# Optimization experiments

Hardware: AMD Instinct MI355X
Metric: run time of the kernel (lower is better)

The kernel has to match this reference:

```python
import jax, jax.numpy as jnp
import numpy as np

B, S, H, DK = 8, 2048, 1024, 64


def setup_inputs() -> dict:
    key = jax.random.key(0)
    ks = jax.random.split(key, 8)
    x = jax.random.normal(ks[0], (B, S, H), dtype=jnp.float32)
    # padding at the tail: positions >= length are pad (True)
    lengths = jax.random.randint(ks[1], (B,), S // 2, S + 1)
    padding_mask = jnp.arange(S)[None, :] >= lengths[:, None]  # [B,S] bool, True = pad
    sc = 1.0 / np.sqrt(H)
    Wq = jax.random.normal(ks[2], (H, DK), dtype=jnp.float32) * sc
    Wk = jax.random.normal(ks[3], (H, DK), dtype=jnp.float32) * sc
    Wv = jax.random.normal(ks[4], (H, DK), dtype=jnp.float32) * sc
    bq = jnp.zeros((DK,), dtype=jnp.float32)
    bk = jnp.zeros((DK,), dtype=jnp.float32)
    bv = jnp.zeros((DK,), dtype=jnp.float32)
    return {"x": x, "padding_mask": padding_mask, "Wq": Wq, "bq": bq,
            "Wk": Wk, "bk": bk, "Wv": Wv, "bv": bv}


def reference(x, padding_mask, Wq, bq, Wk, bk, Wv, bv):
    # Single-head attention, dropout_pe = 0 (identity), masking=True (causal).
    d_k = Wq.shape[-1]
    Q = jnp.einsum('bsh,hd->bsd', x, Wq) + bq
    K = jnp.einsum('bsh,hd->bsd', x, Wk) + bk
    V = jnp.einsum('bsh,hd->bsd', x, Wv) + bv
    scores = jnp.einsum('bqd,bkd->bqk', Q, K) / jnp.sqrt(jnp.asarray(d_k, x.dtype))
    neg_inf = jnp.finfo(scores.dtype).min
    # padding mask over keys: [B,1,S]
    scores = jnp.where(padding_mask[:, None, :], neg_inf, scores)
    # causal mask: strictly upper triangular is disallowed
    seq = scores.shape[-1]
    causal = jnp.triu(jnp.ones((seq, seq), dtype=bool), k=1)
    scores = jnp.where(causal[None, :, :], neg_inf, scores)
    W = jax.nn.softmax(scores, axis=-1)
    # zero out attention rows for padded query positions: [B,S,1]
    W = jnp.where(padding_mask[:, :, None], 0.0, W)
    return jnp.einsum('bqk,bkd->bqd', W, V)
```

## Files before the change

### kernel.cpp

```cpp
#include <hip/hip_runtime.h>
#include <hip/hip_bf16.h>

#define NB 8
#define SEQ 2048
#define HD 1024
#define DK 64

#define QSCALE 0.1803368801111244f
#define FIXMAX2 11.541560327111708f

typedef __attribute__((ext_vector_type(4))) float f32x4;
typedef __attribute__((ext_vector_type(8))) short bf16x8;
typedef __attribute__((ext_vector_type(4))) unsigned short u16x4;

__device__ __forceinline__ short f2bf(float f) {
    union { float f; unsigned u; } v; v.f = f;
    unsigned r = v.u + 0x7fffu + ((v.u >> 16) & 1u);
    return (short)(r >> 16);
}
__device__ __forceinline__ bf16x8 pack8(f32x4 v0, f32x4 v1) {
    union { bf16x8 v; __hip_bfloat162 h[4]; } u;
    u.h[0] = __float22bfloat162_rn(make_float2(v0[0], v0[1]));
    u.h[1] = __float22bfloat162_rn(make_float2(v0[2], v0[3]));
    u.h[2] = __float22bfloat162_rn(make_float2(v1[0], v1[1]));
    u.h[3] = __float22bfloat162_rn(make_float2(v1[2], v1[3]));
    return u.v;
}

__global__ void prep_kernel(const unsigned* __restrict__ mask,
                            const float* __restrict__ Wq, const float* __restrict__ Wk,
                            const float* __restrict__ Wv,
                            int* __restrict__ lengths, short* __restrict__ Wp) {
    if (blockIdx.x < 768) {
        int idx = blockIdx.x * 256 + threadIdx.x;
        int j = idx & 7, lane = (idx >> 3) & 63;
        int slot = idx >> 9;
        int fr = slot % 3, q2 = slot / 3;
        int kh = q2 & 1, cg = (q2 >> 1) & 3, kbg = q2 >> 3;
        int g = lane >> 4, c = lane & 15;
        int n = cg * 3 + fr;
        int m = n >> 2, colm = (n & 3) * 16 + c;
        int k = kbg * 64 + kh * 32 + g * 8 + j;
        const float* W = (m == 0) ? Wq : (m == 1) ? Wk : Wv;
        Wp[idx] = f2bf(W[(size_t)k * DK + colm]);
        return;
    }
    __shared__ int sdet;
    __shared__ int scnt;
    int b = blockIdx.x - 768, t = threadIdx.x;
    if (t == 0) { sdet = 0; scnt = 0; }
    __syncthreads();
    int det = 0;
    for (int i = t; i < 4096; i += 256) {
        unsigned w = mask[i];
        if (w > 1u && w != 0x3F800000u) det = 1;
    }
    if (det) atomicOr(&sdet, 1);
    __syncthreads();
    int cnt = 0;
    if (sdet) {
        const unsigned char* m8 = (const unsigned char*)mask;
        for (int s = t; s < SEQ; s += 256) cnt += (m8[b * SEQ + s] == 0) ? 1 : 0;
    } else {
        for (int s = t; s < SEQ; s += 256) cnt += (mask[b * SEQ + s] == 0u) ? 1 : 0;
    }
    atomicAdd(&scnt, cnt);
    __syncthreads();
    if (t == 0) lengths[b] = scnt;
}

__global__ __launch_bounds__(256, 3) void qkv_kernel(
    const float* __restrict__ x,
    const float* __restrict__ bq, const float* __restrict__ bk, const float* __restrict__ bv,
    const short* __restrict__ Wp,
    short* __restrict__ Q, short* __restrict__ K, short* __restrict__ Vt) {
    __shared__ float xs[2][32][64];
    int t = threadIdx.x;
    int cg = t >> 6, lane = t & 63;
    int g = lane >> 4, c = lane & 15;
    int r0 = blockIdx.x * 32;
    int bb = r0 >> 11, sbase = r0 & (SEQ - 1);

    int srow = t >> 3, sc8 = t & 7;
    const float* xsrc = x + (size_t)(r0 + srow) * HD + sc8 * 8;
    float* wbase = &xs[0][0][0];
    int wo0 = srow * 64 + (((2 * sc8) ^ (srow & 15)) << 2);
    int wo1 = srow * 64 + (((2 * sc8 + 1) ^ (srow & 15)) << 2);

    const short* wpw = Wp + (size_t)cg * 3072 + (size_t)lane * 8;

    f32x4 z = {0.f, 0.f, 0.f, 0.f};
    f32x4 acc[2][3];
    #pragma unroll
    for (int rf = 0; rf < 2; rf++)
        #pragma unroll
        for (int fr = 0; fr < 3; fr++) acc[rf][fr] = z;

    {
        f32x4 x0 = *(const f32x4*)xsrc;
        f32x4 x1 = *(const f32x4*)(xsrc + 4);
        *(f32x4*)(wbase + wo0) = x0;
        *(f32x4*)(wbase + wo1) = x1;
    }
    bf16x8 Bc[2][3];
    #pragma unroll
    for (int kh = 0; kh < 2; kh++)
        #pragma unroll
        for (int fr = 0; fr < 3; fr++)
            Bc[kh][fr] = *(const bf16x8*)(wpw + kh * 1536 + fr * 512);
    f32x4 nxA0 = *(const f32x4*)(xsrc + 64);
    f32x4 nxA1 = *(const f32x4*)(xsrc + 68);
    __syncthreads();

    const float* rbase0 = &xs[0][0][0] + c * 64;
    #pragma unroll
    for (int kbg = 0; kbg < 16; kbg++) {
        int cur = kbg & 1;
        f32x4 nxB0, nxB1;
        bf16x8 Bn[2][3];
        if (kbg < 14) {
            const float* p = xsrc + (kbg + 2) * 64;
            nxB0 = *(const f32x4*)p;
            nxB1 = *(const f32x4*)(p + 4);
        }
        if (kbg < 15) {
            #pragma unroll
            for (int kh = 0; kh < 2; kh++)
                #pragma unroll
                for (int fr = 0; fr < 3; fr++)
                    Bn[kh][fr] = *(const bf16x8*)(wpw + (kbg + 1) * 12288 + kh * 1536 + fr * 512);
        }
        bf16x8 Af[2][2];
        #pragma unroll
        for (int rf = 0; rf < 2; rf++)
            #pragma unroll
            for (int kh = 0; kh < 2; kh++) {
                const float* rp = rbase0 + cur * 2048 + rf * 1024;
                int lg = kh * 8 + 2 * g;
                f32x4 lo = *(const f32x4*)(rp + ((lg ^ c) << 2));
                f32x4 hi = *(const f32x4*)(rp + (((lg + 1) ^ c) << 2));
                Af[rf][kh] = pack8(lo, hi);
            }
        #pragma unroll
        for (int kh = 0; kh < 2; kh++)
            #pragma unroll
            for (int fr = 0; fr < 3; fr++)
                #pragma unroll
                for (int rf = 0; rf < 2; rf++)
                    acc[rf][fr] = __builtin_amdgcn_mfma_f32_16x16x32_bf16(Af[rf][kh], Bc[kh][fr], acc[rf][fr], 0, 0, 0);
        if (kbg < 15) {
            float* wb = wbase + (cur ^ 1) * 2048;
            *(f32x4*)(wb + wo0) = nxA0;
            *(f32x4*)(wb + wo1) = nxA1;
            #pragma unroll
            for (int kh = 0; kh < 2; kh++)
                #pragma unroll
                for (int fr = 0; fr < 3; fr++) Bc[kh][fr] = Bn[kh][fr];
        }
        if (kbg < 14) { nxA0 = nxB0; nxA1 = nxB1; }
        __syncthreads();
    }

    #pragma unroll
    for (int rf = 0; rf < 2; rf++)
        #pragma unroll
        for (int fr = 0; fr < 3; fr++) {
            int n = cg * 3 + fr;
            int m = n >> 2, colm = (n & 3) * 16 + c;
            const float* bias = (m == 0) ? bq : (m == 1) ? bk : bv;
            float bv_ = bias[colm];
            if (m == 2) {
                u16x4 pk;
                #pragma unroll
                for (int j = 0; j < 4; j++) pk[j] = (unsigned short)f2bf(acc[rf][fr][j] + bv_);
                int srw = sbase + rf * 16 + 4 * g;
                *(u16x4*)(Vt + (size_t)bb * DK * SEQ + (size_t)colm * SEQ + srw) = pk;
            } else {
                #pragma unroll
                for (int j = 0; j < 4; j++) {
                    int row = r0 + rf * 16 + 4 * g + j;
                    float s = acc[rf][fr][j] + bv_;
                    if (m == 0) Q[(size_t)row * DK + colm] = f2bf(s * QSCALE);
                    else        K[(size_t)row * DK + colm] = f2bf(s);
                }
            }
        }
}

__global__ __launch_bounds__(256) void attn_kernel(
    const short* __restrict__ Q, const short* __restrict__ K_, const short* __restrict__ Vt,
    const int* __restrict__ lengths, float* __restrict__ out) {
    __shared__ float macc[4][32][66];
    __shared__ float ll[4][32];
    short* plds = (short*)&macc[0][0][0];

    int bid = blockIdx.x;
    int qt = 63 - (bid & 63);
    int b = bid >> 6;
    int len = lengths[b];
    int qbase = qt * 32;
    int t = threadIdx.x;
    int w = t >> 6, lane = t & 63;
    int g = lane >> 4, c = lane & 15;

    if (qbase >= len) {
        int row = t >> 3, seg = t & 7;
        float* op = out + ((size_t)b * SEQ + qbase + row) * DK + seg * 8;
        #pragma unroll
        for (int i = 0; i < 8; i++) op[i] = 0.f;
        return;
    }

    int kend = min(len, qbase + 32);
    int ntiles = (kend + 63) >> 6;
    const short* Qb = Q + ((size_t)b * SEQ + qbase) * DK;
    const short* Kb = K_ + (size_t)b * SEQ * DK;
    const short* Vb = Vt + (size_t)b * DK * SEQ;

    bf16x8 qa[2][2];
    #pragma unroll
    for (int f = 0; f < 2; f++)
        #pragma unroll
        for (int kh = 0; kh < 2; kh++)
            qa[f][kh] = *(const bf16x8*)(Qb + (f * 16 + c) * DK + kh * 32 + g * 8);

    int rowcap[2][4];
    #pragma unroll
    for (int f = 0; f < 2; f++)
        #pragma unroll
        for (int j = 0; j < 4; j++)
            rowcap[f][j] = min(qbase + f * 16 + 4 * g + j, len - 1);

    f32x4 z = {0.f, 0.f, 0.f, 0.f};
    f32x4 acc[2][4];
    float l_r[2][4];
    #pragma unroll
    for (int f = 0; f < 2; f++) {
        #pragma unroll
        for (int n = 0; n < 4; n++) acc[f][n] = z;
        #pragma unroll
        for (int j = 0; j < 4; j++) l_r[f][j] = 0.f;
    }

    short* pldsw = plds + w * 2240;

    bf16x8 kh0[2][2];
    if (w < ntiles) {
        #pragma unroll
        for (int kt = 0; kt < 2; kt++) {
            const short* kp = Kb + (size_t)(w * 64 + kt * 16 + c) * DK + g * 8;
            kh0[kt][0] = *(const bf16x8*)kp;
            kh0[kt][1] = *(const bf16x8*)(kp + 32);
        }
    }

    for (int tt = w; tt < ntiles; tt += 4) {
        int kb = tt * 64;
        bf16x8 kh1[2][2];
        #pragma unroll
        for (int kt = 0; kt < 2; kt++) {
            const short* kp = Kb + (size_t)(kb + 32 + kt * 16 + c) * DK + g * 8;
            kh1[kt][0] = *(const bf16x8*)kp;
            kh1[kt][1] = *(const bf16x8*)(kp + 32);
        }
        f32x4 sf[2][4];
        #pragma unroll
        for (int kt = 0; kt < 2; kt++)
            #pragma unroll
            for (int f = 0; f < 2; f++) {
                f32x4 t0 = __builtin_amdgcn_mfma_f32_16x16x32_bf16(qa[f][0], kh0[kt][0], z, 0, 0, 0);
                sf[f][kt] = __builtin_amdgcn_mfma_f32_16x16x32_bf16(qa[f][1], kh0[kt][1], t0, 0, 0, 0);
            }
        if (tt + 4 < ntiles) {
            #pragma unroll
            for (int kt = 0; kt < 2; kt++) {
                const short* kp = Kb + (size_t)((tt + 4) * 64 + kt * 16 + c) * DK + g * 8;
                kh0[kt][0] = *(const bf16x8*)kp;
                kh0[kt][1] = *(const bf16x8*)(kp + 32);
            }
        }
        bf16x8 vr[4][2];
        #pragma unroll
        for (int n = 0; n < 4; n++) {
            const short* vp = Vb + (size_t)(n * 16 + c) * SEQ + kb + g * 8;
            vr[n][0] = *(const bf16x8*)vp;
            vr[n][1] = *(const bf16x8*)(vp + 32);
        }
        #pragma unroll
        for (int kt = 0; kt < 2; kt++)
            #pragma unroll
            for (int f = 0; f < 2; f++) {
                f32x4 t0 = __builtin_amdgcn_mfma_f32_16x16x32_bf16(qa[f][0], kh1[kt][0], z, 0, 0, 0);
                sf[f][kt + 2] = __builtin_amdgcn_mfma_f32_16x16x32_bf16(qa[f][1], kh1[kt][1], t0, 0, 0, 0);
            }
        #pragma unroll
        for (int kt = 0; kt < 4; kt++) {
            int key = kb + kt * 16 + c;
            #pragma unroll
            for (int f = 0; f < 2; f++)
                #pragma unroll
                for (int j = 0; j < 4; j++) {
                    float s = (key > rowcap[f][j]) ? -1e30f : sf[f][kt][j];
                    float p = exp2f(s - FIXMAX2);
                    sf[f][kt][j] = p;
                    l_r[f][j] += p;
                }
        }
        #pragma unroll
        for (int f = 0; f < 2; f++)
            #pragma unroll
            for (int kt = 0; kt < 4; kt++)
                #pragma unroll
                for (int j = 0; j < 4; j++)
                    pldsw[f * 1120 + (4 * g + j) * 70 + kt * 16 + c] = f2bf(sf[f][kt][j]);
        #pragma unroll
        for (int f = 0; f < 2; f++) {
            bf16x8 pa0 = *(const bf16x8*)(pldsw + f * 1120 + c * 70 + g * 8);
            bf16x8 pa1 = *(const bf16x8*)(pldsw + f * 1120 + c * 70 + 32 + g * 8);
            #pragma unroll
            for (int n = 0; n < 4; n++) {
                acc[f][n] = __builtin_amdgcn_mfma_f32_16x16x32_bf16(pa0, vr[n][0], acc[f][n], 0, 0, 0);
                acc[f][n] = __builtin_amdgcn_mfma_f32_16x16x32_bf16(pa1, vr[n][1], acc[f][n], 0, 0, 0);
            }
        }
    }

    #pragma unroll
    for (int d = 1; d < 16; d <<= 1)
        #pragma unroll
        for (int f = 0; f < 2; f++)
            #pragma unroll
            for (int j = 0; j < 4; j++) l_r[f][j] += __shfl_xor(l_r[f][j], d);

    __syncthreads();
    #pragma unroll
    for (int f = 0; f < 2; f++)
        #pragma unroll
        for (int n = 0; n < 4; n++)
            #pragma unroll
            for (int j = 0; j < 4; j++)
                macc[w][f * 16 + 4 * g + j][n * 16 + c] = acc[f][n][j];
    if (c == 0) {
        #pragma unroll
        for (int f = 0; f < 2; f++)
            #pragma unroll
            for (int j = 0; j < 4; j++)
                ll[w][f * 16 + 4 * g + j] = l_r[f][j];
    }
    __syncthreads();
    {
        int row = t >> 3, seg = t & 7;
        int r = qbase + row;
        float* op = out + ((size_t)b * SEQ + r) * DK + seg * 8;
        float o[8];
        #pragma unroll
        for (int i = 0; i < 8; i++) o[i] = 0.f;
        if (r < len) {
            float L = ll[0][row] + ll[1][row] + ll[2][row] + ll[3][row];
            #pragma unroll
            for (int wv = 0; wv < 4; wv++)
                #pragma unroll
                for (int i = 0; i < 8; i++) o[i] += macc[wv][row][seg * 8 + i];
            float inv = 1.f / L;
            #pragma unroll
            for (int i = 0; i < 8; i++) o[i] *= inv;
        }
        #pragma unroll
        for (int i = 0; i < 8; i++) op[i] = o[i];
    }
}

extern "C" void kernel_launch(void* const* d_in, const int* in_sizes, int n_in,
                              void* d_out, int out_size, void* d_ws, size_t ws_size,
                              hipStream_t stream) {
    const float* x  = (const float*)d_in[0];
    const unsigned* mask = (const unsigned*)d_in[1];
    const float* Wq = (const float*)d_in[2];
    const float* bq = (const float*)d_in[3];
    const float* Wk = (const float*)d_in[4];
    const float* bk = (const float*)d_in[5];
    const float* Wv = (const float*)d_in[6];
    const float* bv = (const float*)d_in[7];
    float* out = (float*)d_out;

    char* ws = (char*)d_ws;
    int*   lengths = (int*)ws;
    short* Wp = (short*)(ws + 256);
    short* Q  = (short*)(ws + 393472);
    short* K  = (short*)(ws + 2490624);
    short* Vt = (short*)(ws + 4587776);

    hipLaunchKernelGGL(prep_kernel, dim3(776), dim3(256), 0, stream, mask, Wq, Wk, Wv, lengths, Wp);
    hipLaunchKernelGGL(qkv_kernel, dim3(512), dim3(256), 0, stream,
                       x, bq, bk, bv, Wp, Q, K, Vt);
    hipLaunchKernelGGL(attn_kernel, dim3(NB * 64), dim3(256), 0, stream,
                       Q, K, Vt, lengths, out);
}
```

Before: 60.94 us.

## Stage x tile as bf16 in LDS, lighten barriers, interleave attention batch order

The QKV projection now converts each thread's x chunk to bf16 before writing it to shared memory, so the LDS tile halves in size and each MFMA A-fragment is one 16-byte LDS read with no per-iteration pack. The swizzle is reworked for the 8-element bf16 chunks. __syncthreads is replaced by an inline s_waitcnt lgkmcnt(0) plus s_barrier, and the occupancy hint on launch_bounds is dropped. The attention grid mapping interleaves batches so that heavy causal tiles from every batch are scheduled first and spread across CUs, which could improve load balance but changes the cache locality of K/V per batch.

```diff
diff --git a/kernel.cpp b/kernel.cpp
--- a/kernel.cpp
+++ b/kernel.cpp
@@ -12,6 +12,8 @@
 typedef __attribute__((ext_vector_type(4))) float f32x4;
 typedef __attribute__((ext_vector_type(8))) short bf16x8;
 typedef __attribute__((ext_vector_type(4))) unsigned short u16x4;
+
+#define LDS_BARRIER() asm volatile("s_waitcnt lgkmcnt(0)\n\ts_barrier" ::: "memory")
 
 __device__ __forceinline__ short f2bf(float f) {
     union { float f; unsigned u; } v; v.f = f;
@@ -69,23 +71,22 @@
     if (t == 0) lengths[b] = scnt;
 }
 
-__global__ __launch_bounds__(256, 3) void qkv_kernel(
+__global__ __launch_bounds__(256) void qkv_kernel(
     const float* __restrict__ x,
     const float* __restrict__ bq, const float* __restrict__ bk, const float* __restrict__ bv,
     const short* __restrict__ Wp,
     short* __restrict__ Q, short* __restrict__ K, short* __restrict__ Vt) {
-    __shared__ float xs[2][32][64];
+    __shared__ short xs[2][32][64];
     int t = threadIdx.x;
     int cg = t >> 6, lane = t & 63;
     int g = lane >> 4, c = lane & 15;
     int r0 = blockIdx.x * 32;
     int bb = r0 >> 11, sbase = r0 & (SEQ - 1);
 
-    int srow = t >> 3, sc8 = t & 7;
-    const float* xsrc = x + (size_t)(r0 + srow) * HD + sc8 * 8;
-    float* wbase = &xs[0][0][0];
-    int wo0 = srow * 64 + (((2 * sc8) ^ (srow & 15)) << 2);
-    int wo1 = srow * 64 + (((2 * sc8 + 1) ^ (srow & 15)) << 2);
+    int srow = t >> 3, ch = t & 7;
+    const float* xsrc = x + (size_t)(r0 + srow) * HD + ch * 8;
+    short* wbase = &xs[0][0][0];
+    int wo = srow * 64 + ((ch ^ (srow & 7)) << 3);
 
     const short* wpw = Wp + (size_t)cg * 3072 + (size_t)lane * 8;
 
@@ -99,8 +100,7 @@
     {
         f32x4 x0 = *(const f32x4*)xsrc;
         f32x4 x1 = *(const f32x4*)(xsrc + 4);
-        *(f32x4*)(wbase + wo0) = x0;
-        *(f32x4*)(wbase + wo1) = x1;
+        *(bf16x8*)(wbase + wo) = pack8(x0, x1);
     }
     bf16x8 Bc[2][3];
     #pragma unroll
@@ -110,9 +110,9 @@
             Bc[kh][fr] = *(const bf16x8*)(wpw + kh * 1536 + fr * 512);
     f32x4 nxA0 = *(const f32x4*)(xsrc + 64);
     f32x4 nxA1 = *(const f32x4*)(xsrc + 68);
-    __syncthreads();
-
-    const float* rbase0 = &xs[0][0][0] + c * 64;
+    LDS_BARRIER();
+
+    const short* rbase0 = &xs[0][0][0] + c * 64;
     #pragma unroll
     for (int kbg = 0; kbg < 16; kbg++) {
         int cur = kbg & 1;
@@ -134,13 +134,9 @@
         #pragma unroll
         for (int rf = 0; rf < 2; rf++)
             #pragma unroll
-            for (int kh = 0; kh < 2; kh++) {
-                const float* rp = rbase0 + cur * 2048 + rf * 1024;
-                int lg = kh * 8 + 2 * g;
-                f32x4 lo = *(const f32x4*)(rp + ((lg ^ c) << 2));
-                f32x4 hi = *(const f32x4*)(rp + (((lg + 1) ^ c) << 2));
-                Af[rf][kh] = pack8(lo, hi);
-            }
+            for (int kh = 0; kh < 2; kh++)
+                Af[rf][kh] = *(const bf16x8*)(rbase0 + cur * 2048 + rf * 1024
+                                              + (((kh * 4 + g) ^ (c & 7)) << 3));
         #pragma unroll
         for (int kh = 0; kh < 2; kh++)
             #pragma unroll
@@ -149,16 +145,14 @@
                 for (int rf = 0; rf < 2; rf++)
                     acc[rf][fr] = __builtin_amdgcn_mfma_f32_16x16x32_bf16(Af[rf][kh], Bc[kh][fr], acc[rf][fr], 0, 0, 0);
         if (kbg < 15) {
-            float* wb = wbase + (cur ^ 1) * 2048;
-            *(f32x4*)(wb + wo0) = nxA0;
-            *(f32x4*)(wb + wo1) = nxA1;
+            *(bf16x8*)(wbase + (cur ^ 1) * 2048 + wo) = pack8(nxA0, nxA1);
             #pragma unroll
             for (int kh = 0; kh < 2; kh++)
                 #pragma unroll
                 for (int fr = 0; fr < 3; fr++) Bc[kh][fr] = Bn[kh][fr];
         }
         if (kbg < 14) { nxA0 = nxB0; nxA1 = nxB1; }
-        __syncthreads();
+        LDS_BARRIER();
     }
 
     #pragma unroll
@@ -195,8 +189,8 @@
     short* plds = (short*)&macc[0][0][0];
 
     int bid = blockIdx.x;
-    int qt = 63 - (bid & 63);
-    int b = bid >> 6;
+    int b = bid & 7;
+    int qt = 63 - (bid >> 3);
     int len = lengths[b];
     int qbase = qt * 32;
     int t = threadIdx.x;
```

After: 58.06 us. 4.7% less time.
